# Optimization experiments

Hardware: AMD Instinct MI355X
Metric: run time of the kernel (lower is better)

## Reference

```python
import jax, jax.numpy as jnp
import numpy as np

GAMMA = 2.0

def _bce_with_logits(x, y):
    # stable: max(x,0) - x*y + log(1+exp(-|x|)) == logaddexp(0,x) - x*y
    return jnp.logaddexp(0.0, x) - x * y

def setup_inputs() -> dict:
    key = jax.random.key(0)
    k1, k2, k3 = jax.random.split(key, 3)
    B = 4_000_000
    logit = jax.random.normal(k1, (B, 7), dtype=jnp.float32)
    label = jax.random.randint(k2, (B,), 0, 2, dtype=jnp.int32)
    repr_mask = jax.random.randint(k3, (B, 7), 0, 2, dtype=jnp.int32)
    return {"logit": logit, "label": label, "repr_mask": repr_mask}

def reference(logit, label, repr_mask):
    B = logit.shape[0]
    logit = logit.reshape(B, -1)                     # [B,7]
    lab = label.astype(logit.dtype)[:, None]         # [B,1], broadcasts like repeat(1,7)
    bce = _bce_with_logits(logit, lab)               # [B,7]
    focal = (1.0 - jnp.exp(-bce)) ** GAMMA * bce
    bce_neg = _bce_with_logits(-logit, 1.0 - lab)
    focal_neg = (1.0 - jnp.exp(-bce_neg)) ** GAMMA * bce_neg
    m = repr_mask.astype(logit.dtype)                # 1 on repr indices
    pos = jnp.sum(focal * m, axis=1)                 # sum over repr_num[i]
    neg = jnp.sum(focal_neg * (1.0 - m), axis=1)     # sum over not_repr
    is_neg_label = (label == 0)
    loss = pos + jnp.where(is_neg_label, neg, jnp.zeros_like(neg))
    return loss
```

## Files before the change

### kernel.cpp

```cpp
#include <hip/hip_runtime.h>


#define TPB 256

__device__ __forceinline__ void focal_both(float x, float& f0, float& f1) {
    float a  = fabsf(x);
    float e  = __expf(-a);
    float r  = __builtin_amdgcn_rcpf(1.0f + e);
    float q  = e * r;
    float Lg = __logf(1.0f + e);
    float tr = q * q * Lg;
    float tq = r * r * (a + Lg);
    bool xpos = (x >= 0.0f);
    f1 = xpos ? tr : tq;
    f0 = xpos ? tq : tr;
}

__global__ __launch_bounds__(TPB, 8) void focal_loss_kernel(
    const float* __restrict__ logit,
    const int*   __restrict__ label,
    const int*   __restrict__ repr_mask,
    float*       __restrict__ out,
    int B)
{
    __shared__ float2 sA[4][448];
    __shared__ float2 sB[4][192];

    const int tid = threadIdx.x;
    const int L   = tid & 63;
    const int w   = tid >> 6;
    const int wc  = blockIdx.x * 4 + w;
    const long R0 = (long)wc * 256;

    float2* A  = sA[w];
    float2* Bc = sB[w];

    if (R0 + 256 <= B) {
        const uint4* lg4 = reinterpret_cast<const uint4*>(logit)     + (size_t)wc * 448;
        const uint4* mk4 = reinterpret_cast<const uint4*>(repr_mask) + (size_t)wc * 448;
        int4 lab4 = reinterpret_cast<const int4*>(label)[(size_t)wc * 64 + L];

        int m  = (L * 9363) >> 16;
        int r0 = L - 7 * m;
        int t4 = 4 * r0;
        int mu = t4 - 7 * ((t4 * 9363) >> 16);

        uint4 lgc = lg4[L];
        uint4 mkc = mk4[L];
#pragma unroll
        for (int k = 0; k < 7; ++k) {
            uint4 lgn, mkn;
            if (k < 6) {
                lgn = lg4[(k + 1) * 64 + L];
                mkn = mk4[(k + 1) * 64 + L];
            }
            float4 xf = *reinterpret_cast<float4*>(&lgc);
            float    xs[4] = { xf.x, xf.y, xf.z, xf.w };
            unsigned ms[4] = { mkc.x, mkc.y, mkc.z, mkc.w };

            float A0 = 0.f, A1 = 0.f, B0 = 0.f, B1 = 0.f;
#pragma unroll
            for (int j = 0; j < 4; ++j) {
                float f0, f1;
                focal_both(xs[j], f0, f1);
                float fm = ms[j] ? f1 : 0.0f;
                bool toB = (mu + j) >= 7;
                A0 += toB ? 0.0f : f0;
                B0 += toB ? f0   : 0.0f;
                A1 += toB ? 0.0f : fm;
                B1 += toB ? fm   : 0.0f;
            }
            A[k * 64 + L] = make_float2(A0, A1);
            if (mu >= 4)
                Bc[3 * m + (mu - 4)] = make_float2(B0, B1);

            m += (mu == 3) ? 10 : 9;
            mu += 4; if (mu >= 7) mu -= 7;
            lgc = lgn; mkc = mkn;
        }

        float2 a0 = A[L * 7 + 0];
        float2 a1 = A[L * 7 + 1];
        float2 a2 = A[L * 7 + 2];
        float2 a3 = A[L * 7 + 3];
        float2 a4 = A[L * 7 + 4];
        float2 a5 = A[L * 7 + 5];
        float2 a6 = A[L * 7 + 6];
        float2 b0 = Bc[L * 3 + 0];
        float2 b1 = Bc[L * 3 + 1];
        float2 b2 = Bc[L * 3 + 2];

        float t0_0 = a0.x + a1.x;             float t1_0 = a0.y + a1.y;
        float t0_1 = b0.x + a2.x + a3.x;      float t1_1 = b0.y + a2.y + a3.y;
        float t0_2 = b1.x + a4.x + a5.x;      float t1_2 = b1.y + a4.y + a5.y;
        float t0_3 = b2.x + a6.x;             float t1_3 = b2.y + a6.y;

        float4 res;
        res.x = (lab4.x != 0) ? t1_0 : t0_0;
        res.y = (lab4.y != 0) ? t1_1 : t0_1;
        res.z = (lab4.z != 0) ? t1_2 : t0_2;
        res.w = (lab4.w != 0) ? t1_3 : t0_3;
        reinterpret_cast<float4*>(out)[(size_t)wc * 64 + L] = res;
    } else if (R0 < B) {
        long r4 = R0 / 4 + L;
        long Q  = B >> 2;
        if (r4 < Q) {
            float res[4];
#pragma unroll
            for (int rr = 0; rr < 4; ++rr) {
                long row = r4 * 4 + rr;
                bool yy = (label[row] != 0);
                float tot = 0.f, ms = 0.f;
                for (int c = 0; c < 7; ++c) {
                    float f0, f1;
                    focal_both(logit[(size_t)row * 7 + c], f0, f1);
                    tot += f0;
                    ms  += repr_mask[(size_t)row * 7 + c] ? f1 : 0.f;
                }
                res[rr] = yy ? ms : tot;
            }
            reinterpret_cast<float4*>(out)[r4] =
                make_float4(res[0], res[1], res[2], res[3]);
        }
    }

    if ((B & 3) && blockIdx.x == 0 && tid == 0) {
        for (long row = (long)(B >> 2) * 4; row < B; ++row) {
            bool yy = (label[row] != 0);
            float tot = 0.f, ms = 0.f;
            for (int c = 0; c < 7; ++c) {
                float f0, f1;
                focal_both(logit[(size_t)row * 7 + c], f0, f1);
                tot += f0;
                ms  += repr_mask[(size_t)row * 7 + c] ? f1 : 0.f;
            }
            out[row] = yy ? ms : tot;
        }
    }
}

extern "C" void kernel_launch(void* const* d_in, const int* in_sizes, int n_in,
                              void* d_out, int out_size, void* d_ws, size_t ws_size,
                              hipStream_t stream) {
    const float* logit     = (const float*)d_in[0];
    const int*   label     = (const int*)d_in[1];
    const int*   repr_mask = (const int*)d_in[2];
    float*       out       = (float*)d_out;

    int B = in_sizes[1];
    long chunks = ((long)B + 255) / 256;
    int blocks = (int)((chunks + 3) / 4);
    if (blocks < 1) blocks = 1;

    focal_loss_kernel<<<blocks, TPB, 0, stream>>>(logit, label, repr_mask, out, B);
}
```

Baseline: 44.11 us.

## Process two chunks per wave with a three-deep cross-chunk prefetch pipeline

Each wave now handles two consecutive 256-row chunks instead of one, which halves the grid size. Loads use a three-slot register ring buffer that prefetches two phases ahead. The first chunk's final phases already prefetch the second chunk's data, so memory latency overlaps across the chunk boundary. The cost is fewer waves in flight, more register pressure from the extra buffered uint4 loads, and duplicated code for the second chunk.

```diff
diff --git a/kernel.cpp b/kernel.cpp
--- a/kernel.cpp
+++ b/kernel.cpp
@@ -16,6 +16,70 @@
     f0 = xpos ? tq : tr;
 }
 
+#define PHASE(lgc, mkc)                                              \
+    {                                                                \
+        float4 xf = *reinterpret_cast<float4*>(&(lgc));              \
+        float    xs[4] = { xf.x, xf.y, xf.z, xf.w };                 \
+        unsigned msx[4] = { (mkc).x, (mkc).y, (mkc).z, (mkc).w };    \
+        float A0=0.f, A1=0.f, B0=0.f, B1=0.f;                        \
+        _Pragma("unroll")                                            \
+        for (int j = 0; j < 4; ++j) {                                \
+            float f0, f1; focal_both(xs[j], f0, f1);                 \
+            float fm = msx[j] ? f1 : 0.0f;                           \
+            bool toB = (mu + j) >= 7;                                \
+            A0 += toB ? 0.0f : f0;  B0 += toB ? f0 : 0.0f;           \
+            A1 += toB ? 0.0f : fm;  B1 += toB ? fm : 0.0f;           \
+        }                                                            \
+        A[k * 64 + L] = make_float2(A0, A1);                         \
+        if (mu >= 4) Bc[3 * m + (mu - 4)] = make_float2(B0, B1);     \
+        m += (mu == 3) ? 10 : 9;                                     \
+        mu += 4; if (mu >= 7) mu -= 7;                               \
+    }
+
+#define COMBINE_STORE(lab4, outIdx)                                  \
+    {                                                                \
+        float2 a0=A[L*7+0], a1=A[L*7+1], a2=A[L*7+2], a3=A[L*7+3],   \
+               a4=A[L*7+4], a5=A[L*7+5], a6=A[L*7+6];                \
+        float2 b0=Bc[L*3+0], b1=Bc[L*3+1], b2=Bc[L*3+2];             \
+        float t00=a0.x+a1.x,      t10=a0.y+a1.y;                     \
+        float t01=b0.x+a2.x+a3.x, t11=b0.y+a2.y+a3.y;                \
+        float t02=b1.x+a4.x+a5.x, t12=b1.y+a4.y+a5.y;                \
+        float t03=b2.x+a6.x,      t13=b2.y+a6.y;                     \
+        float4 res;                                                  \
+        res.x = ((lab4).x != 0) ? t10 : t00;                         \
+        res.y = ((lab4).y != 0) ? t11 : t01;                         \
+        res.z = ((lab4).z != 0) ? t12 : t02;                         \
+        res.w = ((lab4).w != 0) ? t13 : t03;                         \
+        reinterpret_cast<float4*>(out)[(outIdx)] = res;              \
+    }
+
+__device__ __forceinline__ void partial_chunk(
+    long R0, int B, int L,
+    const float* __restrict__ logit, const int* __restrict__ label,
+    const int* __restrict__ repr_mask, float* __restrict__ out)
+{
+    long r4 = R0 / 4 + L;
+    long Q  = (long)B >> 2;
+    if (r4 < Q && r4 * 4 >= R0 && r4 * 4 < R0 + 256) {
+        float res[4];
+#pragma unroll
+        for (int rr = 0; rr < 4; ++rr) {
+            long row = r4 * 4 + rr;
+            bool yy = (label[row] != 0);
+            float tot = 0.f, ms = 0.f;
+            for (int c = 0; c < 7; ++c) {
+                float f0, f1;
+                focal_both(logit[(size_t)row * 7 + c], f0, f1);
+                tot += f0;
+                ms  += repr_mask[(size_t)row * 7 + c] ? f1 : 0.f;
+            }
+            res[rr] = yy ? ms : tot;
+        }
+        reinterpret_cast<float4*>(out)[r4] =
+            make_float4(res[0], res[1], res[2], res[3]);
+    }
+}
+
 __global__ __launch_bounds__(TPB, 8) void focal_loss_kernel(
     const float* __restrict__ logit,
     const int*   __restrict__ label,
@@ -29,99 +93,71 @@
     const int tid = threadIdx.x;
     const int L   = tid & 63;
     const int w   = tid >> 6;
-    const int wc  = blockIdx.x * 4 + w;
-    const long R0 = (long)wc * 256;
-
     float2* A  = sA[w];
     float2* Bc = sB[w];
 
-    if (R0 + 256 <= B) {
-        const uint4* lg4 = reinterpret_cast<const uint4*>(logit)     + (size_t)wc * 448;
-        const uint4* mk4 = reinterpret_cast<const uint4*>(repr_mask) + (size_t)wc * 448;
-        int4 lab4 = reinterpret_cast<const int4*>(label)[(size_t)wc * 64 + L];
+    const long c0 = ((long)blockIdx.x * 4 + w) * 2;
+    const long c1 = c0 + 1;
+    const long R0 = c0 * 256;
+    const long R1 = c1 * 256;
 
-        int m  = (L * 9363) >> 16;
-        int r0 = L - 7 * m;
-        int t4 = 4 * r0;
-        int mu = t4 - 7 * ((t4 * 9363) >> 16);
+    const int m_init  = (L * 9363) >> 16;
+    const int r0i     = L - 7 * m_init;
+    const int t4      = 4 * r0i;
+    const int mu_init = t4 - 7 * ((t4 * 9363) >> 16);
 
-        uint4 lgc = lg4[L];
-        uint4 mkc = mk4[L];
+    const bool full0 = (R0 + 256 <= (long)B);
+    const bool full1 = (R1 + 256 <= (long)B);
+
+    if (full0) {
+        const uint4* lgA = reinterpret_cast<const uint4*>(logit)     + (size_t)c0 * 448;
+        const uint4* mkA = reinterpret_cast<const uint4*>(repr_mask) + (size_t)c0 * 448;
+        const uint4* lgB = reinterpret_cast<const uint4*>(logit)     + (size_t)c1 * 448;
+        const uint4* mkB = reinterpret_cast<const uint4*>(repr_mask) + (size_t)c1 * 448;
+
+        uint4 plg[3], pmk[3];
+        plg[0] = lgA[0 * 64 + L]; pmk[0] = mkA[0 * 64 + L];
+        plg[1] = lgA[1 * 64 + L]; pmk[1] = mkA[1 * 64 + L];
+        int4 lab0 = reinterpret_cast<const int4*>(label)[c0 * 64 + L];
+        int4 lab1 = make_int4(0, 0, 0, 0);
+
+        int m = m_init, mu = mu_init;
 #pragma unroll
         for (int k = 0; k < 7; ++k) {
-            uint4 lgn, mkn;
-            if (k < 6) {
-                lgn = lg4[(k + 1) * 64 + L];
-                mkn = mk4[(k + 1) * 64 + L];
+            if (k + 2 <= 6) {
+                plg[(k + 2) % 3] = lgA[(k + 2) * 64 + L];
+                pmk[(k + 2) % 3] = mkA[(k + 2) * 64 + L];
+            } else if (full1) {
+                plg[(k + 2) % 3] = lgB[(k - 5) * 64 + L];
+                pmk[(k + 2) % 3] = mkB[(k - 5) * 64 + L];
             }
-            float4 xf = *reinterpret_cast<float4*>(&lgc);
-            float    xs[4] = { xf.x, xf.y, xf.z, xf.w };
-            unsigned ms[4] = { mkc.x, mkc.y, mkc.z, mkc.w };
+            if (k == 3 && full1)
+                lab1 = reinterpret_cast<const int4*>(label)[c1 * 64 + L];
 
-            float A0 = 0.f, A1 = 0.f, B0 = 0.f, B1 = 0.f;
+            uint4 lgc = plg[k % 3];
+            uint4 mkc = pmk[k % 3];
+            PHASE(lgc, mkc);
+        }
+        COMBINE_STORE(lab0, (size_t)c0 * 64 + L);
+
+        if (full1) {
+            m = m_init; mu = mu_init;
 #pragma unroll
-            for (int j = 0; j < 4; ++j) {
-                float f0, f1;
-                focal_both(xs[j], f0, f1);
-                float fm = ms[j] ? f1 : 0.0f;
-                bool toB = (mu + j) >= 7;
-                A0 += toB ? 0.0f : f0;
-                B0 += toB ? f0   : 0.0f;
-                A1 += toB ? 0.0f : fm;
-                B1 += toB ? fm   : 0.0f;
+            for (int k = 0; k < 7; ++k) {
+                if (k + 2 <= 6) {
+                    plg[k % 3] = lgB[(k + 2) * 64 + L];
+                    pmk[k % 3] = mkB[(k + 2) * 64 + L];
+                }
+                uint4 lgc = plg[(k + 1) % 3];
+                uint4 mkc = pmk[(k + 1) % 3];
+                PHASE(lgc, mkc);
             }
-            A[k * 64 + L] = make_float2(A0, A1);
-            if (mu >= 4)
-                Bc[3 * m + (mu - 4)] = make_float2(B0, B1);
-
-            m += (mu == 3) ? 10 : 9;
-            mu += 4; if (mu >= 7) mu -= 7;
-            lgc = lgn; mkc = mkn;
+            COMBINE_STORE(lab1, (size_t)c1 * 64 + L);
+        } else if (R1 < (long)B) {
+            partial_chunk(R1, B, L, logit, label, repr_mask, out);
         }
-
-        float2 a0 = A[L * 7 + 0];
-        float2 a1 = A[L * 7 + 1];
-        float2 a2 = A[L * 7 + 2];
-        float2 a3 = A[L * 7 + 3];
-        float2 a4 = A[L * 7 + 4];
-        float2 a5 = A[L * 7 + 5];
-        float2 a6 = A[L * 7 + 6];
-        float2 b0 = Bc[L * 3 + 0];
-        float2 b1 = Bc[L * 3 + 1];
-        float2 b2 = Bc[L * 3 + 2];
-
-        float t0_0 = a0.x + a1.x;             float t1_0 = a0.y + a1.y;
-        float t0_1 = b0.x + a2.x + a3.x;      float t1_1 = b0.y + a2.y + a3.y;
-        float t0_2 = b1.x + a4.x + a5.x;      float t1_2 = b1.y + a4.y + a5.y;
-        float t0_3 = b2.x + a6.x;             float t1_3 = b2.y + a6.y;
-
-        float4 res;
-        res.x = (lab4.x != 0) ? t1_0 : t0_0;
-        res.y = (lab4.y != 0) ? t1_1 : t0_1;
-        res.z = (lab4.z != 0) ? t1_2 : t0_2;
-        res.w = (lab4.w != 0) ? t1_3 : t0_3;
-        reinterpret_cast<float4*>(out)[(size_t)wc * 64 + L] = res;
-    } else if (R0 < B) {
-        long r4 = R0 / 4 + L;
-        long Q  = B >> 2;
-        if (r4 < Q) {
-            float res[4];
-#pragma unroll
-            for (int rr = 0; rr < 4; ++rr) {
-                long row = r4 * 4 + rr;
-                bool yy = (label[row] != 0);
-                float tot = 0.f, ms = 0.f;
-                for (int c = 0; c < 7; ++c) {
-                    float f0, f1;
-                    focal_both(logit[(size_t)row * 7 + c], f0, f1);
-                    tot += f0;
-                    ms  += repr_mask[(size_t)row * 7 + c] ? f1 : 0.f;
-                }
-                res[rr] = yy ? ms : tot;
-            }
-            reinterpret_cast<float4*>(out)[r4] =
-                make_float4(res[0], res[1], res[2], res[3]);
-        }
+    } else if (R0 < (long)B) {
+        partial_chunk(R0, B, L, logit, label, repr_mask, out);
     }
 
     if ((B & 3) && blockIdx.x == 0 && tid == 0) {
@@ -149,7 +185,8 @@
 
     int B = in_sizes[1];
     long chunks = ((long)B + 255) / 256;
-    int blocks = (int)((chunks + 3) / 4);
+    long slots  = (chunks + 1) / 2;
+    int blocks  = (int)((slots + 3) / 4);
     if (blocks < 1) blocks = 1;
 
     focal_loss_kernel<<<blocks, TPB, 0, stream>>>(logit, label, repr_mask, out, B);
```

Result: slower. 52.27 us (+18.5%).
